# Optimization experiments

Hardware: AMD Instinct MI355X
Metric: run time of the kernel (lower is better)

The kernel has to match this reference:

```python
import jax, jax.numpy as jnp
import numpy as np
from jax import lax

D_MODEL = 512
D_FIBER = 32
D_CONTROL = 64
MOMENTUM = 0.9


def setup_inputs() -> dict:
    key = jax.random.key(0)
    ks = jax.random.split(key, 7)
    B, S = 8, 4096
    hidden = jax.random.normal(ks[0], (B, S, D_MODEL), dtype=jnp.float32)
    # fiber_proj: Linear(d_model -> d_fiber)
    w_fiber = jax.random.normal(ks[1], (D_MODEL, D_FIBER), dtype=jnp.float32) / np.sqrt(D_MODEL)
    b_fiber = jnp.zeros((D_FIBER,), dtype=jnp.float32)
    # predictor: Linear(d_model+d_fiber -> d_control), GELU, Linear(d_control -> 1), Softplus
    w1 = jax.random.normal(ks[2], (D_MODEL + D_FIBER, D_CONTROL), dtype=jnp.float32) / np.sqrt(D_MODEL + D_FIBER)
    b1 = jnp.zeros((D_CONTROL,), dtype=jnp.float32)
    # nn.init.normal_(weight, std=0.01), zero bias for the last linear
    w2 = 0.01 * jax.random.normal(ks[3], (D_CONTROL, 1), dtype=jnp.float32)
    b2 = jnp.zeros((1,), dtype=jnp.float32)
    lambda_gate = jnp.asarray(1.0, dtype=jnp.float32)
    return {"hidden": hidden, "w_fiber": w_fiber, "b_fiber": b_fiber,
            "w1": w1, "b1": b1, "w2": w2, "b2": b2, "lambda_gate": lambda_gate}


def _ema_scan(delta_h, momentum):
    # field_t = momentum * field_{t-1} + (1-momentum) * delta_h_t, field_{-1}=0.
    # Same math as the original full-length causal conv1d (Toeplitz) form,
    # computed in O(S log S) via an associative scan.
    a = jnp.full_like(delta_h, momentum)
    b = (1.0 - momentum) * delta_h

    def combine(c1, c2):
        a1, b1 = c1
        a2, b2 = c2
        return (a1 * a2, a2 * b1 + b2)

    _, field = lax.associative_scan(combine, (a, b), axis=1)
    return field


def reference(hidden, w_fiber, b_fiber, w1, b1, w2, b2, lambda_gate):
    # hidden: [B, S, D]
    fiber = hidden @ w_fiber + b_fiber                      # [B, S, d_fiber]
    combined = jnp.concatenate([hidden, fiber], axis=-1)    # [B, S, D+d_fiber]
    h = jax.nn.gelu(combined @ w1 + b1, approximate=False)  # [B, S, d_control]
    delta_h = jax.nn.softplus((h @ w2 + b2).squeeze(-1))    # [B, S]
    delta_h = jnp.clip(delta_h, 0.0, 1.0)
    field = _ema_scan(delta_h, MOMENTUM)                    # [B, S]
    field = jnp.clip(field, 0.0, 10.0)
    gate = jax.nn.sigmoid(-lambda_gate * field)             # [B, S]
    return (gate, field, delta_h, fiber)
```

## Files before the change

### kernel.cpp

```cpp
#include <hip/hip_runtime.h>
#include <hip/hip_bf16.h>


#define NTOK  32768
#define SEQ   4096
#define DM    512
#define NC    96
#define TB    64
#define KC    128
#define LROW  136

typedef short bf16x8 __attribute__((ext_vector_type(8)));
typedef float f32x4  __attribute__((ext_vector_type(4)));

__device__ __forceinline__ unsigned short f2bf(float f) {
    __hip_bfloat16 h = __float2bfloat16(f);
    return *reinterpret_cast<unsigned short*>(&h);
}

__global__ __launch_bounds__(256)
void prep_kernel(const float* __restrict__ wf,
                 const float* __restrict__ bfb,
                 const float* __restrict__ w1,
                 const float* __restrict__ b1,
                 unsigned short* __restrict__ Wt,
                 float* __restrict__ bc)
{
    int idx = blockIdx.x * 256 + threadIdx.x;
    if (idx < NC * DM) {
        int n = idx >> 9, k = idx & 511;
        float v;
        if (n < 32) {
            v = wf[k * 32 + n];
        } else {
            int c = n - 32;
            v = w1[k * 64 + c];
            for (int f = 0; f < 32; ++f)
                v = fmaf(wf[k * 32 + f], w1[(512 + f) * 64 + c], v);
        }
        Wt[idx] = f2bf(v);
    }
    if (idx < NC) {
        float v;
        if (idx < 32) {
            v = bfb[idx];
        } else {
            int c = idx - 32;
            v = b1[c];
            for (int f = 0; f < 32; ++f)
                v = fmaf(bfb[f], w1[(512 + f) * 64 + c], v);
        }
        bc[idx] = v;
    }
}

__global__ __launch_bounds__(256, 2)
void fused_gemm_kernel(const float* __restrict__ hidden,
                       const unsigned short* __restrict__ Wt,
                       const float* __restrict__ bc,
                       const float* __restrict__ w2,
                       const float* __restrict__ b2,
                       float* __restrict__ out_delta,
                       float* __restrict__ out_fiber)
{
    __shared__ unsigned short a_lds[TB * LROW];
    __shared__ unsigned short b_lds[NC * LROW];

    const int tid  = threadIdx.x;
    const int wave = tid >> 6;
    const int lane = tid & 63;
    const int quad = lane >> 4;
    const int l15  = lane & 15;
    const int tok0 = blockIdx.x * TB;

    f32x4 acc[6];
#pragma unroll
    for (int t = 0; t < 6; ++t) acc[t] = (f32x4){0.f, 0.f, 0.f, 0.f};

    for (int kc = 0; kc < DM; kc += KC) {
#pragma unroll
        for (int it = 0; it < 8; ++it) {
            int v   = it * 256 + tid;
            int row = v >> 5;
            int c4  = v & 31;
            float4 u = *(const float4*)(hidden + (size_t)(tok0 + row) * DM + kc + c4 * 4);
            ushort4 o;
            o.x = f2bf(u.x); o.y = f2bf(u.y); o.z = f2bf(u.z); o.w = f2bf(u.w);
            *(ushort4*)&a_lds[row * LROW + c4 * 4] = o;
        }
#pragma unroll
        for (int it = 0; it < 6; ++it) {
            int v   = it * 256 + tid;
            int row = v >> 4;
            int c8  = v & 15;
            bf16x8 u = *(const bf16x8*)(Wt + row * DM + kc + c8 * 8);
            *(bf16x8*)&b_lds[row * LROW + c8 * 8] = u;
        }
        __syncthreads();

#pragma unroll
        for (int ks = 0; ks < 4; ++ks) {
            bf16x8 af = *(const bf16x8*)&a_lds[(wave * 16 + l15) * LROW + ks * 32 + quad * 8];
#pragma unroll
            for (int t = 0; t < 6; ++t) {
                bf16x8 bfv = *(const bf16x8*)&b_lds[(t * 16 + l15) * LROW + ks * 32 + quad * 8];
                acc[t] = __builtin_amdgcn_mfma_f32_16x16x32_bf16(af, bfv, acc[t], 0, 0, 0);
            }
        }
        __syncthreads();
    }

    const int mbase = tok0 + wave * 16 + quad * 4;

#pragma unroll
    for (int t = 0; t < 2; ++t) {
        int col = t * 16 + l15;
        float bias = bc[col];
#pragma unroll
        for (int r = 0; r < 4; ++r)
            out_fiber[(size_t)(mbase + r) * 32 + col] = acc[t][r] + bias;
    }

    float p0 = 0.f, p1 = 0.f, p2 = 0.f, p3 = 0.f;
#pragma unroll
    for (int t = 2; t < 6; ++t) {
        int c = (t - 2) * 16 + l15;
        float bias = bc[32 + c];
        float w2v  = w2[c];
        float x, g;
        x = acc[t][0] + bias; g = 0.5f * x * (1.f + erff(x * 0.70710678118f)); p0 = fmaf(g, w2v, p0);
        x = acc[t][1] + bias; g = 0.5f * x * (1.f + erff(x * 0.70710678118f)); p1 = fmaf(g, w2v, p1);
        x = acc[t][2] + bias; g = 0.5f * x * (1.f + erff(x * 0.70710678118f)); p2 = fmaf(g, w2v, p2);
        x = acc[t][3] + bias; g = 0.5f * x * (1.f + erff(x * 0.70710678118f)); p3 = fmaf(g, w2v, p3);
    }
#pragma unroll
    for (int m = 1; m <= 8; m <<= 1) {
        p0 += __shfl_xor(p0, m);
        p1 += __shfl_xor(p1, m);
        p2 += __shfl_xor(p2, m);
        p3 += __shfl_xor(p3, m);
    }
    if (l15 < 4) {
        float pv = (l15 == 0) ? p0 : (l15 == 1) ? p1 : (l15 == 2) ? p2 : p3;
        float s = pv + b2[0];
        float d = (s > 0.f) ? s + log1pf(expf(-s)) : log1pf(expf(s));
        d = fminf(fmaxf(d, 0.f), 1.f);
        out_delta[mbase + l15] = d;
    }
}

__global__ __launch_bounds__(256)
void scan_kernel(const float* __restrict__ delta,
                 const float* __restrict__ lam,
                 float* __restrict__ out_gate,
                 float* __restrict__ out_field)
{
    __shared__ float lds_d[512];
    const int b     = blockIdx.x >> 4;
    const int chunk = blockIdx.x & 15;
    const int s0    = chunk * 256;
    const int tid   = threadIdx.x;

    for (int v = tid; v < 512; v += 256) {
        int s = s0 - 256 + v;
        lds_d[v] = (s >= 0) ? delta[b * SEQ + s] : 0.f;
    }
    __syncthreads();

    float w = 0.1f, acc = 0.f;
    const int base = 256 + tid;
    for (int j = 0; j < 256; ++j) {
        acc = fmaf(w, lds_d[base - j], acc);
        w *= 0.9f;
    }
    float field = fminf(fmaxf(acc, 0.f), 10.f);

    float gate = 1.f / (1.f + expf(lam[0] * field));
    int t = b * SEQ + s0 + tid;
    out_field[t] = field;
    out_gate[t]  = gate;
}

extern "C" void kernel_launch(void* const* d_in, const int* in_sizes, int n_in,
                              void* d_out, int out_size, void* d_ws, size_t ws_size,
                              hipStream_t stream)
{
    const float* hidden = (const float*)d_in[0];
    const float* wf     = (const float*)d_in[1];
    const float* bfb    = (const float*)d_in[2];
    const float* w1     = (const float*)d_in[3];
    const float* b1     = (const float*)d_in[4];
    const float* w2     = (const float*)d_in[5];
    const float* b2     = (const float*)d_in[6];
    const float* lam    = (const float*)d_in[7];
    float* out = (float*)d_out;
    float* out_gate  = out;
    float* out_field = out + NTOK;
    float* out_delta = out + 2 * NTOK;
    float* out_fiber = out + 3 * NTOK;

    unsigned short* Wt = (unsigned short*)d_ws;
    float* bc          = (float*)((char*)d_ws + NC * DM * 2);

    hipLaunchKernelGGL(prep_kernel, dim3((NC * DM + 255) / 256), dim3(256), 0, stream,
                       wf, bfb, w1, b1, Wt, bc);
    hipLaunchKernelGGL(fused_gemm_kernel, dim3(NTOK / TB), dim3(256), 0, stream,
                       hidden, Wt, bc, w2, b2, out_delta, out_fiber);
    hipLaunchKernelGGL(scan_kernel, dim3(128), dim3(256), 0, stream,
                       out_delta, lam, out_gate, out_field);
}
```

Measured before the change: 117.7 us.

## Load A operand straight to registers, shorten scan window, split scan accumulators

The GEMM kernel stops staging hidden activations through LDS. Each lane loads its own fp32 row slice directly into registers and converts it to bf16 MFMA fragments, while the B tile loads are issued ahead of the A loads and stored to LDS afterwards. The scan kernel cuts the truncated EMA window from 256 to 128 taps and uses four independent accumulators to break the FMA dependency chain. The prep kernel vectorizes the fiber-weight loads. The direct A loads are less coalesced, and the shorter scan window drops tail terms of order 0.9^128, which are negligible.

```diff
diff --git a/kernel.cpp b/kernel.cpp
--- a/kernel.cpp
+++ b/kernel.cpp
@@ -16,6 +16,15 @@
 __device__ __forceinline__ unsigned short f2bf(float f) {
     __hip_bfloat16 h = __float2bfloat16(f);
     return *reinterpret_cast<unsigned short*>(&h);
+}
+
+__device__ __forceinline__ bf16x8 cvt8(float4 u, float4 v) {
+    bf16x8 r;
+    r[0] = (short)f2bf(u.x); r[1] = (short)f2bf(u.y);
+    r[2] = (short)f2bf(u.z); r[3] = (short)f2bf(u.w);
+    r[4] = (short)f2bf(v.x); r[5] = (short)f2bf(v.y);
+    r[6] = (short)f2bf(v.z); r[7] = (short)f2bf(v.w);
+    return r;
 }
 
 __global__ __launch_bounds__(256)
@@ -35,8 +44,15 @@
         } else {
             int c = n - 32;
             v = w1[k * 64 + c];
-            for (int f = 0; f < 32; ++f)
-                v = fmaf(wf[k * 32 + f], w1[(512 + f) * 64 + c], v);
+            const float4* wfr = (const float4*)(wf + k * 32);
+#pragma unroll
+            for (int f4 = 0; f4 < 8; ++f4) {
+                float4 u = wfr[f4];
+                v = fmaf(u.x, w1[(512 + f4 * 4 + 0) * 64 + c], v);
+                v = fmaf(u.y, w1[(512 + f4 * 4 + 1) * 64 + c], v);
+                v = fmaf(u.z, w1[(512 + f4 * 4 + 2) * 64 + c], v);
+                v = fmaf(u.w, w1[(512 + f4 * 4 + 3) * 64 + c], v);
+            }
         }
         Wt[idx] = f2bf(v);
     }
@@ -63,7 +79,6 @@
                        float* __restrict__ out_delta,
                        float* __restrict__ out_fiber)
 {
-    __shared__ unsigned short a_lds[TB * LROW];
     __shared__ unsigned short b_lds[NC * LROW];
 
     const int tid  = threadIdx.x;
@@ -73,38 +88,44 @@
     const int l15  = lane & 15;
     const int tok0 = blockIdx.x * TB;
 
+    const float* arow = hidden + (size_t)(tok0 + wave * 16 + l15) * DM + quad * 8;
+
     f32x4 acc[6];
 #pragma unroll
     for (int t = 0; t < 6; ++t) acc[t] = (f32x4){0.f, 0.f, 0.f, 0.f};
 
+#pragma unroll 1
     for (int kc = 0; kc < DM; kc += KC) {
-#pragma unroll
-        for (int it = 0; it < 8; ++it) {
-            int v   = it * 256 + tid;
-            int row = v >> 5;
-            int c4  = v & 31;
-            float4 u = *(const float4*)(hidden + (size_t)(tok0 + row) * DM + kc + c4 * 4);
-            ushort4 o;
-            o.x = f2bf(u.x); o.y = f2bf(u.y); o.z = f2bf(u.z); o.w = f2bf(u.w);
-            *(ushort4*)&a_lds[row * LROW + c4 * 4] = o;
-        }
+        bf16x8 breg[6];
 #pragma unroll
         for (int it = 0; it < 6; ++it) {
-            int v   = it * 256 + tid;
-            int row = v >> 4;
-            int c8  = v & 15;
-            bf16x8 u = *(const bf16x8*)(Wt + row * DM + kc + c8 * 8);
-            *(bf16x8*)&b_lds[row * LROW + c8 * 8] = u;
+            int v = it * 256 + tid;
+            breg[it] = *(const bf16x8*)(Wt + (v >> 4) * DM + kc + (v & 15) * 8);
+        }
+        float4 a[8];
+#pragma unroll
+        for (int ks = 0; ks < 4; ++ks) {
+            const float* ap = arow + kc + ks * 32;
+            a[2 * ks]     = *(const float4*)ap;
+            a[2 * ks + 1] = *(const float4*)(ap + 4);
+        }
+#pragma unroll
+        for (int it = 0; it < 6; ++it) {
+            int v = it * 256 + tid;
+            *(bf16x8*)&b_lds[(v >> 4) * LROW + (v & 15) * 8] = breg[it];
         }
         __syncthreads();
 
+        bf16x8 af[4];
+#pragma unroll
+        for (int ks = 0; ks < 4; ++ks) af[ks] = cvt8(a[2 * ks], a[2 * ks + 1]);
+
 #pragma unroll
         for (int ks = 0; ks < 4; ++ks) {
-            bf16x8 af = *(const bf16x8*)&a_lds[(wave * 16 + l15) * LROW + ks * 32 + quad * 8];
 #pragma unroll
             for (int t = 0; t < 6; ++t) {
                 bf16x8 bfv = *(const bf16x8*)&b_lds[(t * 16 + l15) * LROW + ks * 32 + quad * 8];
-                acc[t] = __builtin_amdgcn_mfma_f32_16x16x32_bf16(af, bfv, acc[t], 0, 0, 0);
+                acc[t] = __builtin_amdgcn_mfma_f32_16x16x32_bf16(af[ks], bfv, acc[t], 0, 0, 0);
             }
         }
         __syncthreads();
@@ -155,25 +176,30 @@
                  float* __restrict__ out_gate,
                  float* __restrict__ out_field)
 {
-    __shared__ float lds_d[512];
+    __shared__ float lds_d[384];
     const int b     = blockIdx.x >> 4;
     const int chunk = blockIdx.x & 15;
     const int s0    = chunk * 256;
     const int tid   = threadIdx.x;
 
-    for (int v = tid; v < 512; v += 256) {
-        int s = s0 - 256 + v;
+    for (int v = tid; v < 384; v += 256) {
+        int s = s0 - 128 + v;
         lds_d[v] = (s >= 0) ? delta[b * SEQ + s] : 0.f;
     }
     __syncthreads();
 
-    float w = 0.1f, acc = 0.f;
-    const int base = 256 + tid;
-    for (int j = 0; j < 256; ++j) {
-        acc = fmaf(w, lds_d[base - j], acc);
-        w *= 0.9f;
-    }
-    float field = fminf(fmaxf(acc, 0.f), 10.f);
+    const int base = 128 + tid;
+    const float r4 = 0.6561f;
+    float w0 = 0.1f, w1v = 0.09f, w2v = 0.081f, w3v = 0.0729f;
+    float p0 = 0.f, p1 = 0.f, p2 = 0.f, p3 = 0.f;
+#pragma unroll
+    for (int j = 0; j < 128; j += 4) {
+        p0 = fmaf(w0,  lds_d[base - j],     p0); w0  *= r4;
+        p1 = fmaf(w1v, lds_d[base - j - 1], p1); w1v *= r4;
+        p2 = fmaf(w2v, lds_d[base - j - 2], p2); w2v *= r4;
+        p3 = fmaf(w3v, lds_d[base - j - 3], p3); w3v *= r4;
+    }
+    float field = fminf(fmaxf((p0 + p1) + (p2 + p3), 0.f), 10.f);
 
     float gate = 1.f / (1.f + expf(lam[0] * field));
     int t = b * SEQ + s0 + tid;
```

Measured after the change: 120.2 us. 2.2% more time.
